# Optimization experiments

Hardware: AMD Instinct MI355X
Metric: run time of the kernel (lower is better)

## Reference

```python
import jax, jax.numpy as jnp
import numpy as np

BSZ, NW, T = 16, 1024, 3072   # batch, max words per seq, padded byte length
BED, WED = 128, 512           # byte_embed_dim, word_embed_dim
NH = 2                        # highway layers per block
VOCAB = 256 + 4 + 4
BPE_MASK_IDX = 4


def _conv1d(x, W, b):
    # x: [B, T, Cin], W: [k, Cin, Cout]
    y = jax.lax.conv_general_dilated(x, W, window_strides=(1,), padding='SAME',
                                     dimension_numbers=('NWC', 'WIO', 'NWC'))
    return y + b


def _highway(x, Ws, bs):
    # Ws: [NH, 2D, D], bs: [NH, 2D]; AllenNLP-style highway
    for i in range(NH):
        proj = x @ Ws[i].T + bs[i]
        h, g = jnp.split(proj, 2, axis=-1)
        g = jax.nn.sigmoid(g)
        x = g * jax.nn.relu(h) + (1.0 - g) * x
    return x


def setup_inputs() -> dict:
    rng = np.random.default_rng(0)
    pool_lengths = rng.integers(1, 4, size=(BSZ, NW)).astype(np.int64)  # all >=1 -> npools == NW
    src_lengths = pool_lengths.sum(axis=1)
    byte_tokens = np.zeros((BSZ, T), dtype=np.int64)
    for b in range(BSZ):
        L = int(src_lengths[b])
        byte_tokens[b, :L] = rng.integers(4, 260, size=L)
    pos = np.arange(T)[None, :]
    bpe_mask = (rng.random((BSZ, T)) < 0.3) & (pos < src_lengths[:, None])

    key = jax.random.key(0)
    ks = jax.random.split(key, 12)
    s = 0.02
    tok_emb = jax.random.normal(ks[0], (VOCAB, BED), jnp.float32) * s
    tok_emb = tok_emb.at[0].set(0.0)  # padding_idx = 0
    return {
        'byte_tokens': jnp.asarray(byte_tokens),
        'bpe_mask': jnp.asarray(bpe_mask),
        'pool_lengths': jnp.asarray(pool_lengths),
        'tok_emb': tok_emb,
        'conv0_W': jax.random.normal(ks[1], (3, BED, WED), jnp.float32) * s,
        'conv0_b': jnp.zeros((WED,), jnp.float32),
        'conv1_W': jax.random.normal(ks[2], (3, WED, WED), jnp.float32) * s,
        'conv1_b': jnp.zeros((WED,), jnp.float32),
        'hw0_W': jax.random.normal(ks[3], (NH, 2 * WED, WED), jnp.float32) * s,
        'hw0_b': jnp.zeros((NH, 2 * WED), jnp.float32),
        'hw1_W': jax.random.normal(ks[4], (NH, 2 * WED, WED), jnp.float32) * s,
        'hw1_b': jnp.zeros((NH, 2 * WED), jnp.float32),
        'proj_W': jax.random.normal(ks[5], (WED, WED), jnp.float32) * s,
        'proj_b': jnp.zeros((WED,), jnp.float32),
    }


def reference(byte_tokens, bpe_mask, pool_lengths, tok_emb,
              conv0_W, conv0_b, conv1_W, conv1_b,
              hw0_W, hw0_b, hw1_W, hw1_b, proj_W, proj_b):
    # byte embedding + bpe-marker embedding (index 0 row is zero => no-op where mask is False)
    x = tok_emb[byte_tokens] + tok_emb[jnp.where(bpe_mask, BPE_MASK_IDX, 0)]
    # ConvHighway block 0 (no residual)
    x = _highway(jax.nn.relu(_conv1d(x, conv0_W, conv0_b)), hw0_W, hw0_b)
    # ConvHighway block 1 (residual_conv=True); dropout is identity in eval
    x = _highway(jax.nn.relu(_conv1d(x, conv1_W, conv1_b)) + x, hw1_W, hw1_b)

    # ragged per-word max pool via segment_max (replaces the python double loop)
    cum = jnp.cumsum(pool_lengths, axis=1)                 # [B, NW]
    pos = jnp.arange(T)
    seg = jax.vmap(lambda c: jnp.searchsorted(c, pos, side='right'))(cum)  # [B, T]
    src_len = cum[:, -1]
    valid = pos[None, :] < src_len[:, None]
    gid = jnp.where(valid, jnp.arange(BSZ)[:, None] * NW + jnp.clip(seg, 0, NW - 1), BSZ * NW)
    pooled = jax.ops.segment_max(x.reshape(BSZ * T, WED), gid.reshape(-1),
                                 num_segments=BSZ * NW + 1)
    pooled = pooled[:BSZ * NW].reshape(BSZ, NW, WED)
    pooled = jnp.where(jnp.isfinite(pooled), pooled, 0.0)  # empty pools -> 0 like new_zeros
    return pooled @ proj_W.T + proj_b
```

## Files before the change

kernel.cpp:

```cpp
#include <hip/hip_runtime.h>
#include <hip/hip_bf16.h>
#include <math.h>

typedef __attribute__((ext_vector_type(8))) short short8v;
typedef __attribute__((ext_vector_type(4))) float float4v;

namespace {
constexpr int kBSZ = 16;
constexpr int kNW  = 1024;
constexpr int kT   = 3072;
constexpr int kBED = 128;
constexpr int kWED = 512;
constexpr int kR   = kBSZ * kT;
constexpr int kMP  = kBSZ * kNW;
}

__device__ __forceinline__ unsigned short f2b(float x) {
  unsigned int u = __float_as_uint(x);
  u = u + 0x7FFFu + ((u >> 16) & 1u);
  return (unsigned short)(u >> 16);
}
__device__ __forceinline__ float b2f(unsigned short u) {
  return __uint_as_float(((unsigned int)u) << 16);
}

__device__ __forceinline__ void async16(void* l, const void* g) {
  __builtin_amdgcn_global_load_lds(
      (const __attribute__((address_space(1))) void*)g,
      (__attribute__((address_space(3))) void*)l, 16, 0, 0);
}

__device__ __forceinline__ int swz(int row) { return (row >> 1) & 3; }

__global__ __launch_bounds__(256) void k_embed(
    const int* __restrict__ tok, const int* __restrict__ msk,
    const float* __restrict__ emb, unsigned short* __restrict__ out) {
  int idx = blockIdx.x * 256 + threadIdx.x;
  int row = idx >> 5, c4 = idx & 31;
  const float4* e4 = (const float4*)emb;
  float4 a = e4[tok[row] * 32 + c4];
  float4 b = e4[(msk[row] ? 4 : 0) * 32 + c4];
  ushort4 o;
  o.x = f2b(a.x + b.x); o.y = f2b(a.y + b.y);
  o.z = f2b(a.z + b.z); o.w = f2b(a.w + b.w);
  ((ushort4*)out)[idx] = o;
}

__global__ __launch_bounds__(256) void k_prep(
    const float* __restrict__ c0W, const float* __restrict__ c1W,
    const float* __restrict__ h0W, const float* __restrict__ h1W,
    const float* __restrict__ pW,
    unsigned short* __restrict__ cw0, unsigned short* __restrict__ cw1,
    unsigned short* __restrict__ hw0, unsigned short* __restrict__ hw1,
    unsigned short* __restrict__ pwb) {
  int idx = blockIdx.x * 256 + threadIdx.x;
  if (idx < 196608) {
    int k = idx & 127, n = (idx >> 7) & 511, dt = idx >> 16;
    cw0[idx] = f2b(c0W[(long)(dt * 128 + k) * 512 + n]);
    return;
  }
  idx -= 196608;
  if (idx < 786432) {
    int k = idx & 511, n = (idx >> 9) & 511, dt = idx >> 18;
    cw1[idx] = f2b(c1W[(long)(dt * 512 + k) * 512 + n]);
    return;
  }
  idx -= 786432;
  if (idx < 1048576) { hw0[idx] = f2b(h0W[idx]); return; }
  idx -= 1048576;
  if (idx < 1048576) { hw1[idx] = f2b(h1W[idx]); return; }
  idx -= 1048576;
  if (idx < 262144)  { pwb[idx] = f2b(pW[idx]); }
}

__global__ void k_cumsum(const int* __restrict__ pl, int* __restrict__ cum) {
  __shared__ int s[kNW];
  int b = blockIdx.x, i = threadIdx.x;
  s[i] = pl[b * kNW + i];
  __syncthreads();
  for (int off = 1; off < kNW; off <<= 1) {
    int cur = s[i];
    int add = (i >= off) ? s[i - off] : 0;
    __syncthreads();
    s[i] = cur + add;
    __syncthreads();
  }
  cum[b * kNW + i] = s[i];
}

template <int CIN, bool RESID>
__global__ __launch_bounds__(256, 2) void k_convm(
    const unsigned short* __restrict__ X,
    const unsigned short* __restrict__ Wt,
    const float* __restrict__ bias,
    const unsigned short* __restrict__ resid,
    const int* __restrict__ cum,
    unsigned short* __restrict__ out) {
  const int row0 = blockIdx.x * 128, n0 = blockIdx.y * 128;
  const int b = row0 / kT, t0 = row0 % kT;
  if (t0 >= cum[b * kNW + kNW - 1] + 2) return;

  constexpr int NT = CIN / 32;
  __shared__ short lds[2][(130 + 384) * 32];
  const int tid = threadIdx.x, wave = tid >> 6, lane = tid & 63;
  const int q = lane >> 4, rr = lane & 15;
  const int dr = lane >> 2, sl = lane & 3;
  const bool lo_ok = (t0 > 0), hi_ok = (t0 + 128 < kT);
  const int wr = (wave >> 1) * 64, wc = (wave & 1) * 64;

  float4v acc[4][4] = {};
  short8v hv = {0, 0, 0, 0, 0, 0, 0, 0};
  const int hch = tid & 3;
  const long hrow = (tid < 4) ? (long)(row0 - 1) : (long)(row0 + 128);
  const bool hok = (tid < 4) ? lo_ok : hi_ok;

  auto stage = [&](int nb, int k0) {
    short* As = lds[nb];
    short* Bs = lds[nb] + 130 * 32;
#pragma unroll
    for (int i = 0; i < 2; ++i) {
      int r0 = (wave + 4 * i) * 16;
      int ch = sl ^ swz(1 + r0 + dr);
      async16((char*)As + (1 + r0) * 64,
              X + (long)(row0 + r0 + dr) * CIN + k0 + ch * 8);
    }
#pragma unroll
    for (int i = 0; i < 6; ++i) {
      int r0 = (wave + 4 * i) * 16;
      int br = r0 + dr;
      int ch = sl ^ swz(br);
      int dt = br >> 7, n = br & 127;
      async16((char*)Bs + r0 * 64,
              Wt + ((long)(dt * kWED + n0 + n)) * CIN + k0 + ch * 8);
    }
    if (tid < 8) {
      short8v v = {0, 0, 0, 0, 0, 0, 0, 0};
      if (hok) v = *(const short8v*)(X + hrow * CIN + k0 + hch * 8);
      hv = v;
    }
  };
  auto halo_write = [&](int nb) {
    if (tid < 8) {
      int r = (tid < 4) ? 0 : 129;
      *(short8v*)((char*)lds[nb] + r * 64 + hch * 16) = hv;
    }
  };

  stage(0, 0);
  halo_write(0);
  __syncthreads();

  for (int t = 0; t < NT; ++t) {
    const int cur = t & 1, nb = cur ^ 1;
    if (t + 1 < NT) stage(nb, (t + 1) * 32);
    __builtin_amdgcn_sched_barrier(0);
    const char* As = (const char*)lds[cur];
    const char* Bs = (const char*)(lds[cur] + 130 * 32);
#pragma unroll
    for (int dt = 0; dt < 3; ++dt) {
      short8v a[4], bb[4];
#pragma unroll
      for (int mf = 0; mf < 4; ++mf) {
        int ra = wr + rr + dt + mf * 16;
        a[mf] = *(const short8v*)(As + ra * 64 + ((q ^ swz(ra)) * 16));
      }
#pragma unroll
      for (int nf = 0; nf < 4; ++nf) {
        int rb = dt * 128 + wc + rr + nf * 16;
        bb[nf] = *(const short8v*)(Bs + rb * 64 + ((q ^ swz(rb)) * 16));
      }
#pragma unroll
      for (int mf = 0; mf < 4; ++mf)
#pragma unroll
        for (int nf = 0; nf < 4; ++nf)
          acc[mf][nf] = __builtin_amdgcn_mfma_f32_16x16x32_bf16(
              a[mf], bb[nf], acc[mf][nf], 0, 0, 0);
    }
    if (t + 1 < NT) halo_write(nb);
    __syncthreads();
  }

#pragma unroll
  for (int nf = 0; nf < 4; ++nf) {
    int col = n0 + wc + nf * 16 + rr;
    float bv = bias[col];
#pragma unroll
    for (int mf = 0; mf < 4; ++mf)
#pragma unroll
      for (int r = 0; r < 4; ++r) {
        long row = row0 + wr + mf * 16 + q * 4 + r;
        float y = fmaxf(acc[mf][nf][r] + bv, 0.f);
        if (RESID) y += b2f(resid[row * kWED + col]);
        out[row * kWED + col] = f2b(y);
      }
  }
}

__global__ __launch_bounds__(256, 2) void k_hw(
    const unsigned short* __restrict__ X,
    const unsigned short* __restrict__ Wb,
    const float* __restrict__ bias,
    const int* __restrict__ cum,
    unsigned short* __restrict__ out) {
  const int row0 = blockIdx.x * 128, n0 = blockIdx.y * 128;
  const int b = row0 / kT, t0 = row0 % kT;
  if (t0 >= cum[b * kNW + kNW - 1] + 2) return;

  __shared__ short lds[2][(128 + 256) * 32];
  const int tid = threadIdx.x, wave = tid >> 6, lane = tid & 63;
  const int q = lane >> 4, rr = lane & 15;
  const int dr = lane >> 2, sl = lane & 3;
  const int wr = (wave >> 1) * 64, wc = (wave & 1) * 64;

  float4v acch[4][4] = {}, accg[4][4] = {};

  auto stage = [&](int nb, int k0) {
    short* As = lds[nb];
    short* Bs = lds[nb] + 128 * 32;
#pragma unroll
    for (int i = 0; i < 2; ++i) {
      int r0 = (wave + 4 * i) * 16;
      int ch = sl ^ swz(r0 + dr);
      async16((char*)As + r0 * 64,
              X + (long)(row0 + r0 + dr) * kWED + k0 + ch * 8);
    }
#pragma unroll
    for (int i = 0; i < 4; ++i) {
      int r0 = (wave + 4 * i) * 16;
      int br = r0 + dr;
      int ch = sl ^ swz(br);
      int g = br >> 7, n = br & 127;
      async16((char*)Bs + r0 * 64,
              Wb + ((long)(g * 512 + n0 + n)) * kWED + k0 + ch * 8);
    }
  };

  stage(0, 0);
  __syncthreads();

  for (int t = 0; t < 16; ++t) {
    const int cur = t & 1, nb = cur ^ 1;
    if (t + 1 < 16) stage(nb, (t + 1) * 32);
    __builtin_amdgcn_sched_barrier(0);
    const char* As = (const char*)lds[cur];
    const char* Bs = (const char*)(lds[cur] + 128 * 32);
    short8v a[4], bh[4], bg[4];
#pragma unroll
    for (int mf = 0; mf < 4; ++mf) {
      int ra = wr + rr + mf * 16;
      a[mf] = *(const short8v*)(As + ra * 64 + ((q ^ swz(ra)) * 16));
    }
#pragma unroll
    for (int nf = 0; nf < 4; ++nf) {
      int rh = wc + rr + nf * 16;
      int rg = 128 + rh;
      bh[nf] = *(const short8v*)(Bs + rh * 64 + ((q ^ swz(rh)) * 16));
      bg[nf] = *(const short8v*)(Bs + rg * 64 + ((q ^ swz(rg)) * 16));
    }
#pragma unroll
    for (int mf = 0; mf < 4; ++mf)
#pragma unroll
      for (int nf = 0; nf < 4; ++nf) {
        acch[mf][nf] = __builtin_amdgcn_mfma_f32_16x16x32_bf16(
            a[mf], bh[nf], acch[mf][nf], 0, 0, 0);
        accg[mf][nf] = __builtin_amdgcn_mfma_f32_16x16x32_bf16(
            a[mf], bg[nf], accg[mf][nf], 0, 0, 0);
      }
    __syncthreads();
  }

#pragma unroll
  for (int nf = 0; nf < 4; ++nf) {
    int col = n0 + wc + nf * 16 + rr;
    float bhv = bias[col], bgv = bias[512 + col];
#pragma unroll
    for (int mf = 0; mf < 4; ++mf)
#pragma unroll
      for (int r = 0; r < 4; ++r) {
        long row = row0 + wr + mf * 16 + q * 4 + r;
        float h = fmaxf(acch[mf][nf][r] + bhv, 0.f);
        float g = 1.f / (1.f + __expf(-(accg[mf][nf][r] + bgv)));
        float xv = b2f(X[row * kWED + col]);
        out[row * kWED + col] = f2b(g * h + (1.f - g) * xv);
      }
  }
}

__global__ __launch_bounds__(256, 2) void k_proj(
    const unsigned short* __restrict__ A,
    const unsigned short* __restrict__ Wb,
    const float* __restrict__ bias,
    float* __restrict__ out) {
  __shared__ short lds[2][(128 + 128) * 32];
  const int tid = threadIdx.x, wave = tid >> 6, lane = tid & 63;
  const int q = lane >> 4, rr = lane & 15;
  const int dr = lane >> 2, sl = lane & 3;
  const int row0 = blockIdx.x * 128, n0 = blockIdx.y * 128;
  const int wr = (wave >> 1) * 64, wc = (wave & 1) * 64;

  float4v acc[4][4] = {};

  auto stage = [&](int nb, int k0) {
    short* As = lds[nb];
    short* Bs = lds[nb] + 128 * 32;
#pragma unroll
    for (int i = 0; i < 2; ++i) {
      int r0 = (wave + 4 * i) * 16;
      int ch = sl ^ swz(r0 + dr);
      async16((char*)As + r0 * 64,
              A + (long)(row0 + r0 + dr) * kWED + k0 + ch * 8);
    }
#pragma unroll
    for (int i = 0; i < 2; ++i) {
      int r0 = (wave + 4 * i) * 16;
      int ch = sl ^ swz(r0 + dr);
      async16((char*)Bs + r0 * 64,
              Wb + (long)(n0 + r0 + dr) * kWED + k0 + ch * 8);
    }
  };

  stage(0, 0);
  __syncthreads();

  for (int t = 0; t < 16; ++t) {
    const int cur = t & 1, nb = cur ^ 1;
    if (t + 1 < 16) stage(nb, (t + 1) * 32);
    __builtin_amdgcn_sched_barrier(0);
    const char* As = (const char*)lds[cur];
    const char* Bs = (const char*)(lds[cur] + 128 * 32);
    short8v a[4], bb[4];
#pragma unroll
    for (int mf = 0; mf < 4; ++mf) {
      int ra = wr + rr + mf * 16;
      a[mf] = *(const short8v*)(As + ra * 64 + ((q ^ swz(ra)) * 16));
    }
#pragma unroll
    for (int nf = 0; nf < 4; ++nf) {
      int rb = wc + rr + nf * 16;
      bb[nf] = *(const short8v*)(Bs + rb * 64 + ((q ^ swz(rb)) * 16));
    }
#pragma unroll
    for (int mf = 0; mf < 4; ++mf)
#pragma unroll
      for (int nf = 0; nf < 4; ++nf)
        acc[mf][nf] = __builtin_amdgcn_mfma_f32_16x16x32_bf16(
            a[mf], bb[nf], acc[mf][nf], 0, 0, 0);
    __syncthreads();
  }

#pragma unroll
  for (int nf = 0; nf < 4; ++nf) {
    int col = n0 + wc + nf * 16 + rr;
    float bv = bias[col];
#pragma unroll
    for (int mf = 0; mf < 4; ++mf)
#pragma unroll
      for (int r = 0; r < 4; ++r) {
        long row = row0 + wr + mf * 16 + q * 4 + r;
        out[row * kWED + col] = acc[mf][nf][r] + bv;
      }
  }
}

__global__ __launch_bounds__(128) void k_pool(
    const unsigned short* __restrict__ x, const int* __restrict__ cum,
    unsigned short* __restrict__ pooled) {
  int bw = blockIdx.x;
  int b = bw >> 10, w = bw & 1023;
  int s = (w == 0) ? 0 : cum[bw - 1];
  int e = cum[bw];
  int c = threadIdx.x;
  float m0 = -INFINITY, m1 = -INFINITY, m2 = -INFINITY, m3 = -INFINITY;
  for (int t = s; t < e; ++t) {
    ushort4 v = ((const ushort4*)(x + (long)(b * kT + t) * kWED))[c];
    m0 = fmaxf(m0, b2f(v.x)); m1 = fmaxf(m1, b2f(v.y));
    m2 = fmaxf(m2, b2f(v.z)); m3 = fmaxf(m3, b2f(v.w));
  }
  if (e <= s) { m0 = m1 = m2 = m3 = 0.f; }
  ushort4 o;
  o.x = f2b(m0); o.y = f2b(m1); o.z = f2b(m2); o.w = f2b(m3);
  ((ushort4*)(pooled + (long)bw * kWED))[c] = o;
}

extern "C" void kernel_launch(void* const* d_in, const int* in_sizes, int n_in,
                              void* d_out, int out_size, void* d_ws, size_t ws_size,
                              hipStream_t stream) {
  (void)in_sizes; (void)n_in; (void)out_size; (void)ws_size;

  const int*   tok = (const int*)d_in[0];
  const int*   msk = (const int*)d_in[1];
  const int*   pl  = (const int*)d_in[2];
  const float* emb = (const float*)d_in[3];
  const float* c0W = (const float*)d_in[4];
  const float* c0b = (const float*)d_in[5];
  const float* c1W = (const float*)d_in[6];
  const float* c1b = (const float*)d_in[7];
  const float* h0W = (const float*)d_in[8];
  const float* h0b = (const float*)d_in[9];
  const float* h1W = (const float*)d_in[10];
  const float* h1b = (const float*)d_in[11];
  const float* pW  = (const float*)d_in[12];
  const float* pb  = (const float*)d_in[13];

  unsigned short* xb0 = (unsigned short*)d_ws;
  unsigned short* xb1 = xb0 + (size_t)kR * kWED;
  unsigned short* cw0 = xb1 + (size_t)kR * kWED;
  unsigned short* cw1 = cw0 + 3 * kWED * kBED;
  unsigned short* hw0 = cw1 + 3 * kWED * kWED;
  unsigned short* hw1 = hw0 + 2 * 1024 * kWED;
  unsigned short* pwb = hw1 + 2 * 1024 * kWED;
  int* cum = (int*)(pwb + kWED * kWED);

  k_cumsum<<<kBSZ, kNW, 0, stream>>>(pl, cum);

  k_prep<<<(3342336 + 255) / 256, 256, 0, stream>>>(
      c0W, c1W, h0W, h1W, pW, cw0, cw1, hw0, hw1, pwb);

  k_embed<<<kR * 32 / 256, 256, 0, stream>>>(tok, msk, emb, xb0);

  dim3 g1(kR / 128, kWED / 128);

  k_convm<kBED, false><<<g1, 256, 0, stream>>>(xb0, cw0, c0b, nullptr, cum, xb1);
  k_hw<<<g1, 256, 0, stream>>>(xb1, hw0, h0b, cum, xb0);
  k_hw<<<g1, 256, 0, stream>>>(xb0, hw0 + 1024 * kWED, h0b + 1024, cum, xb1);
  k_convm<kWED, true><<<g1, 256, 0, stream>>>(xb1, cw1, c1b, xb1, cum, xb0);
  k_hw<<<g1, 256, 0, stream>>>(xb0, hw1, h1b, cum, xb1);
  k_hw<<<g1, 256, 0, stream>>>(xb1, hw1 + 1024 * kWED, h1b + 1024, cum, xb0);

  k_pool<<<kMP, 128, 0, stream>>>(xb0, cum, xb1);

  dim3 g2(kMP / 128, kWED / 128);
  k_proj<<<g2, 256, 0, stream>>>(xb1, pwb, pb, (float*)d_out);
}
```

Baseline: 399.8 us.

## Triple-buffer highway and projection GEMM LDS pipelines with explicit vmcnt waits

Switches the highway and projection GEMM kernels from double to triple buffering in LDS, prefetching two K-steps ahead. Each stage is issued after the current tile's LDS reads, and the loop waits with partial vmcnt counts plus a raw s_barrier instead of a full __syncthreads. The aim is to hide global-load latency behind the MFMA work. In exchange, LDS use per block grows by half (about 72 KB for k_hw), which may cut the number of resident blocks, and correctness depends on the hand-counted vmcnt values.

```diff
diff --git a/kernel.cpp b/kernel.cpp
--- a/kernel.cpp
+++ b/kernel.cpp
@@ -4,6 +4,9 @@
 
 typedef __attribute__((ext_vector_type(8))) short short8v;
 typedef __attribute__((ext_vector_type(4))) float float4v;
+
+#define VMCNT(n) asm volatile("s_waitcnt vmcnt(" #n ")" ::: "memory")
+#define LGK0     asm volatile("s_waitcnt lgkmcnt(0)" ::: "memory")
 
 namespace {
 constexpr int kBSZ = 16;
@@ -206,7 +209,7 @@
   const int b = row0 / kT, t0 = row0 % kT;
   if (t0 >= cum[b * kNW + kNW - 1] + 2) return;
 
-  __shared__ short lds[2][(128 + 256) * 32];
+  __shared__ short lds[3][(128 + 256) * 32];
   const int tid = threadIdx.x, wave = tid >> 6, lane = tid & 63;
   const int q = lane >> 4, rr = lane & 15;
   const int dr = lane >> 2, sl = lane & 3;
@@ -236,14 +239,14 @@
   };
 
   stage(0, 0);
-  __syncthreads();
+  stage(1, 32);
+  VMCNT(6);
+  __builtin_amdgcn_s_barrier();
+  __builtin_amdgcn_sched_barrier(0);
 
   for (int t = 0; t < 16; ++t) {
-    const int cur = t & 1, nb = cur ^ 1;
-    if (t + 1 < 16) stage(nb, (t + 1) * 32);
-    __builtin_amdgcn_sched_barrier(0);
-    const char* As = (const char*)lds[cur];
-    const char* Bs = (const char*)(lds[cur] + 128 * 32);
+    const char* As = (const char*)lds[t % 3];
+    const char* Bs = (const char*)(lds[t % 3] + 128 * 32);
     short8v a[4], bh[4], bg[4];
 #pragma unroll
     for (int mf = 0; mf < 4; ++mf) {
@@ -257,6 +260,8 @@
       bh[nf] = *(const short8v*)(Bs + rh * 64 + ((q ^ swz(rh)) * 16));
       bg[nf] = *(const short8v*)(Bs + rg * 64 + ((q ^ swz(rg)) * 16));
     }
+    if (t + 2 < 16) stage((t + 2) % 3, (t + 2) * 32);
+    LGK0; __builtin_amdgcn_sched_barrier(0);
 #pragma unroll
     for (int mf = 0; mf < 4; ++mf)
 #pragma unroll
@@ -266,7 +271,9 @@
         accg[mf][nf] = __builtin_amdgcn_mfma_f32_16x16x32_bf16(
             a[mf], bg[nf], accg[mf][nf], 0, 0, 0);
       }
-    __syncthreads();
+    if (t + 2 < 16) { VMCNT(6); } else { VMCNT(0); }
+    __builtin_amdgcn_s_barrier();
+    __builtin_amdgcn_sched_barrier(0);
   }
 
 #pragma unroll
@@ -291,7 +298,7 @@
     const unsigned short* __restrict__ Wb,
     const float* __restrict__ bias,
     float* __restrict__ out) {
-  __shared__ short lds[2][(128 + 128) * 32];
+  __shared__ short lds[3][(128 + 128) * 32];
   const int tid = threadIdx.x, wave = tid >> 6, lane = tid & 63;
   const int q = lane >> 4, rr = lane & 15;
   const int dr = lane >> 2, sl = lane & 3;
@@ -320,14 +327,14 @@
   };
 
   stage(0, 0);
-  __syncthreads();
+  stage(1, 32);
+  VMCNT(4);
+  __builtin_amdgcn_s_barrier();
+  __builtin_amdgcn_sched_barrier(0);
 
   for (int t = 0; t < 16; ++t) {
-    const int cur = t & 1, nb = cur ^ 1;
-    if (t + 1 < 16) stage(nb, (t + 1) * 32);
-    __builtin_amdgcn_sched_barrier(0);
-    const char* As = (const char*)lds[cur];
-    const char* Bs = (const char*)(lds[cur] + 128 * 32);
+    const char* As = (const char*)lds[t % 3];
+    const char* Bs = (const char*)(lds[t % 3] + 128 * 32);
     short8v a[4], bb[4];
 #pragma unroll
     for (int mf = 0; mf < 4; ++mf) {
@@ -339,13 +346,17 @@
       int rb = wc + rr + nf * 16;
       bb[nf] = *(const short8v*)(Bs + rb * 64 + ((q ^ swz(rb)) * 16));
     }
+    if (t + 2 < 16) stage((t + 2) % 3, (t + 2) * 32);
+    LGK0; __builtin_amdgcn_sched_barrier(0);
 #pragma unroll
     for (int mf = 0; mf < 4; ++mf)
 #pragma unroll
       for (int nf = 0; nf < 4; ++nf)
         acc[mf][nf] = __builtin_amdgcn_mfma_f32_16x16x32_bf16(
             a[mf], bb[nf], acc[mf][nf], 0, 0, 0);
-    __syncthreads();
+    if (t + 2 < 16) { VMCNT(4); } else { VMCNT(0); }
+    __builtin_amdgcn_s_barrier();
+    __builtin_amdgcn_sched_barrier(0);
   }
 
 #pragma unroll
```

Result: no change. 398.4 us (-0.4%).

## Single-buffer LDS in GEMM kernels and raise occupancy via launch bounds

Applied to the files above, without the earlier changes.

Drops the double-buffered LDS prefetch pipeline in the conv, highway and projection GEMM kernels in favour of a single buffer with load-sync-compute-sync per K step. It also precomputes incrementing global pointers and raises the launch-bounds occupancy targets. The aim is to fit more blocks per CU so wave-level parallelism hides memory latency. In exchange it loses intra-block overlap of loads with MFMA and puts more pressure on registers.

```diff
diff --git a/kernel.cpp b/kernel.cpp
--- a/kernel.cpp
+++ b/kernel.cpp
@@ -89,7 +89,7 @@
 }
 
 template <int CIN, bool RESID>
-__global__ __launch_bounds__(256, 2) void k_convm(
+__global__ __launch_bounds__(256, 4) void k_convm(
     const unsigned short* __restrict__ X,
     const unsigned short* __restrict__ Wt,
     const float* __restrict__ bias,
@@ -101,7 +101,7 @@
   if (t0 >= cum[b * kNW + kNW - 1] + 2) return;
 
   constexpr int NT = CIN / 32;
-  __shared__ short lds[2][(130 + 384) * 32];
+  __shared__ short lds[(130 + 384) * 32];
   const int tid = threadIdx.x, wave = tid >> 6, lane = tid & 63;
   const int q = lane >> 4, rr = lane & 15;
   const int dr = lane >> 2, sl = lane & 3;
@@ -109,53 +109,48 @@
   const int wr = (wave >> 1) * 64, wc = (wave & 1) * 64;
 
   float4v acc[4][4] = {};
-  short8v hv = {0, 0, 0, 0, 0, 0, 0, 0};
+
+  const unsigned short* pA[2];
+  int lA[2];
+#pragma unroll
+  for (int i = 0; i < 2; ++i) {
+    int r0 = (wave + 4 * i) * 16;
+    int ch = sl ^ swz(1 + r0 + dr);
+    pA[i] = X + (long)(row0 + r0 + dr) * CIN + ch * 8;
+    lA[i] = (1 + r0) * 64;
+  }
+  const unsigned short* pB[6];
+  int lB[6];
+#pragma unroll
+  for (int i = 0; i < 6; ++i) {
+    int r0 = (wave + 4 * i) * 16;
+    int br = r0 + dr;
+    int ch = sl ^ swz(br);
+    int dt = br >> 7, n = br & 127;
+    pB[i] = Wt + ((long)(dt * kWED + n0 + n)) * CIN + ch * 8;
+    lB[i] = (130 + r0) * 64;
+  }
   const int hch = tid & 3;
   const long hrow = (tid < 4) ? (long)(row0 - 1) : (long)(row0 + 128);
   const bool hok = (tid < 4) ? lo_ok : hi_ok;
-
-  auto stage = [&](int nb, int k0) {
-    short* As = lds[nb];
-    short* Bs = lds[nb] + 130 * 32;
-#pragma unroll
-    for (int i = 0; i < 2; ++i) {
-      int r0 = (wave + 4 * i) * 16;
-      int ch = sl ^ swz(1 + r0 + dr);
-      async16((char*)As + (1 + r0) * 64,
-              X + (long)(row0 + r0 + dr) * CIN + k0 + ch * 8);
-    }
-#pragma unroll
-    for (int i = 0; i < 6; ++i) {
-      int r0 = (wave + 4 * i) * 16;
-      int br = r0 + dr;
-      int ch = sl ^ swz(br);
-      int dt = br >> 7, n = br & 127;
-      async16((char*)Bs + r0 * 64,
-              Wt + ((long)(dt * kWED + n0 + n)) * CIN + k0 + ch * 8);
-    }
+  const unsigned short* pH = X + hrow * CIN + hch * 8;
+  const int lH = ((tid < 4) ? 0 : 129) * 64 + hch * 16;
+
+  for (int t = 0; t < NT; ++t) {
+#pragma unroll
+    for (int i = 0; i < 2; ++i) { async16((char*)lds + lA[i], pA[i]); pA[i] += 32; }
+#pragma unroll
+    for (int i = 0; i < 6; ++i) { async16((char*)lds + lB[i], pB[i]); pB[i] += 32; }
     if (tid < 8) {
       short8v v = {0, 0, 0, 0, 0, 0, 0, 0};
-      if (hok) v = *(const short8v*)(X + hrow * CIN + k0 + hch * 8);
-      hv = v;
-    }
-  };
-  auto halo_write = [&](int nb) {
-    if (tid < 8) {
-      int r = (tid < 4) ? 0 : 129;
-      *(short8v*)((char*)lds[nb] + r * 64 + hch * 16) = hv;
-    }
-  };
-
-  stage(0, 0);
-  halo_write(0);
-  __syncthreads();
-
-  for (int t = 0; t < NT; ++t) {
-    const int cur = t & 1, nb = cur ^ 1;
-    if (t + 1 < NT) stage(nb, (t + 1) * 32);
-    __builtin_amdgcn_sched_barrier(0);
-    const char* As = (const char*)lds[cur];
-    const char* Bs = (const char*)(lds[cur] + 130 * 32);
+      if (hok) v = *(const short8v*)pH;
+      *(short8v*)((char*)lds + lH) = v;
+    }
+    pH += 32;
+    __syncthreads();
+
+    const char* As = (const char*)lds;
+    const char* Bs = (const char*)(lds + 130 * 32);
 #pragma unroll
     for (int dt = 0; dt < 3; ++dt) {
       short8v a[4], bb[4];
@@ -176,7 +171,6 @@
           acc[mf][nf] = __builtin_amdgcn_mfma_f32_16x16x32_bf16(
               a[mf], bb[nf], acc[mf][nf], 0, 0, 0);
     }
-    if (t + 1 < NT) halo_write(nb);
     __syncthreads();
   }
 
@@ -196,7 +190,7 @@
   }
 }
 
-__global__ __launch_bounds__(256, 2) void k_hw(
+__global__ __launch_bounds__(256, 3) void k_hw(
     const unsigned short* __restrict__ X,
     const unsigned short* __restrict__ Wb,
     const float* __restrict__ bias,
@@ -206,7 +200,7 @@
   const int b = row0 / kT, t0 = row0 % kT;
   if (t0 >= cum[b * kNW + kNW - 1] + 2) return;
 
-  __shared__ short lds[2][(128 + 256) * 32];
+  __shared__ short lds[(128 + 256) * 32];
   const int tid = threadIdx.x, wave = tid >> 6, lane = tid & 63;
   const int q = lane >> 4, rr = lane & 15;
   const int dr = lane >> 2, sl = lane & 3;
@@ -214,37 +208,37 @@
 
   float4v acch[4][4] = {}, accg[4][4] = {};
 
-  auto stage = [&](int nb, int k0) {
-    short* As = lds[nb];
-    short* Bs = lds[nb] + 128 * 32;
-#pragma unroll
-    for (int i = 0; i < 2; ++i) {
-      int r0 = (wave + 4 * i) * 16;
-      int ch = sl ^ swz(r0 + dr);
-      async16((char*)As + r0 * 64,
-              X + (long)(row0 + r0 + dr) * kWED + k0 + ch * 8);
-    }
-#pragma unroll
-    for (int i = 0; i < 4; ++i) {
-      int r0 = (wave + 4 * i) * 16;
-      int br = r0 + dr;
-      int ch = sl ^ swz(br);
-      int g = br >> 7, n = br & 127;
-      async16((char*)Bs + r0 * 64,
-              Wb + ((long)(g * 512 + n0 + n)) * kWED + k0 + ch * 8);
-    }
-  };
-
-  stage(0, 0);
-  __syncthreads();
+  const unsigned short* pA[2];
+  int lA[2];
+#pragma unroll
+  for (int i = 0; i < 2; ++i) {
+    int r0 = (wave + 4 * i) * 16;
+    int ch = sl ^ swz(r0 + dr);
+    pA[i] = X + (long)(row0 + r0 + dr) * kWED + ch * 8;
+    lA[i] = r0 * 64;
+  }
+  const unsigned short* pB[4];
+  int lB[4];
+#pragma unroll
+  for (int i = 0; i < 4; ++i) {
+    int r0 = (wave + 4 * i) * 16;
+    int br = r0 + dr;
+    int ch = sl ^ swz(br);
+    int g = br >> 7, n = br & 127;
+    pB[i] = Wb + ((long)(g * 512 + n0 + n)) * kWED + ch * 8;
+    lB[i] = (128 + r0) * 64;
+  }
 
   for (int t = 0; t < 16; ++t) {
-    const int cur = t & 1, nb = cur ^ 1;
-    if (t + 1 < 16) stage(nb, (t + 1) * 32);
-    __builtin_amdgcn_sched_barrier(0);
-    const char* As = (const char*)lds[cur];
-    const char* Bs = (const char*)(lds[cur] + 128 * 32);
-    short8v a[4], bh[4], bg[4];
+#pragma unroll
+    for (int i = 0; i < 2; ++i) { async16((char*)lds + lA[i], pA[i]); pA[i] += 32; }
+#pragma unroll
+    for (int i = 0; i < 4; ++i) { async16((char*)lds + lB[i], pB[i]); pB[i] += 32; }
+    __syncthreads();
+
+    const char* As = (const char*)lds;
+    const char* Bs = (const char*)(lds + 128 * 32);
+    short8v a[4];
 #pragma unroll
     for (int mf = 0; mf < 4; ++mf) {
       int ra = wr + rr + mf * 16;
@@ -254,18 +248,16 @@
     for (int nf = 0; nf < 4; ++nf) {
       int rh = wc + rr + nf * 16;
       int rg = 128 + rh;
-      bh[nf] = *(const short8v*)(Bs + rh * 64 + ((q ^ swz(rh)) * 16));
-      bg[nf] = *(const short8v*)(Bs + rg * 64 + ((q ^ swz(rg)) * 16));
-    }
-#pragma unroll
-    for (int mf = 0; mf < 4; ++mf)
-#pragma unroll
-      for (int nf = 0; nf < 4; ++nf) {
+      short8v bh = *(const short8v*)(Bs + rh * 64 + ((q ^ swz(rh)) * 16));
+      short8v bg = *(const short8v*)(Bs + rg * 64 + ((q ^ swz(rg)) * 16));
+#pragma unroll
+      for (int mf = 0; mf < 4; ++mf) {
         acch[mf][nf] = __builtin_amdgcn_mfma_f32_16x16x32_bf16(
-            a[mf], bh[nf], acch[mf][nf], 0, 0, 0);
+            a[mf], bh, acch[mf][nf], 0, 0, 0);
         accg[mf][nf] = __builtin_amdgcn_mfma_f32_16x16x32_bf16(
-            a[mf], bg[nf], accg[mf][nf], 0, 0, 0);
-      }
+            a[mf], bg, accg[mf][nf], 0, 0, 0);
+      }
+    }
     __syncthreads();
   }
 
@@ -286,12 +278,12 @@
   }
 }
 
-__global__ __launch_bounds__(256, 2) void k_proj(
+__global__ __launch_bounds__(256, 4) void k_proj(
     const unsigned short* __restrict__ A,
     const unsigned short* __restrict__ Wb,
     const float* __restrict__ bias,
     float* __restrict__ out) {
-  __shared__ short lds[2][(128 + 128) * 32];
+  __shared__ short lds[(128 + 128) * 32];
   const int tid = threadIdx.x, wave = tid >> 6, lane = tid & 63;
   const int q = lane >> 4, rr = lane & 15;
   const int dr = lane >> 2, sl = lane & 3;
@@ -300,34 +292,28 @@
 
   float4v acc[4][4] = {};
 
-  auto stage = [&](int nb, int k0) {
-    short* As = lds[nb];
-    short* Bs = lds[nb] + 128 * 32;
-#pragma unroll
-    for (int i = 0; i < 2; ++i) {
-      int r0 = (wave + 4 * i) * 16;
-      int ch = sl ^ swz(r0 + dr);
-      async16((char*)As + r0 * 64,
-              A + (long)(row0 + r0 + dr) * kWED + k0 + ch * 8);
-    }
-#pragma unroll
-    for (int i = 0; i < 2; ++i) {
-      int r0 = (wave + 4 * i) * 16;
-      int ch = sl ^ swz(r0 + dr);
-      async16((char*)Bs + r0 * 64,
-              Wb + (long)(n0 + r0 + dr) * kWED + k0 + ch * 8);
-    }
-  };
-
-  stage(0, 0);
-  __syncthreads();
+  const unsigned short* pA[2];
+  const unsigned short* pB[2];
+  int lA[2], lB[2];
+#pragma unroll
+  for (int i = 0; i < 2; ++i) {
+    int r0 = (wave + 4 * i) * 16;
+    int ch = sl ^ swz(r0 + dr);
+    pA[i] = A + (long)(row0 + r0 + dr) * kWED + ch * 8;
+    lA[i] = r0 * 64;
+    pB[i] = Wb + (long)(n0 + r0 + dr) * kWED + ch * 8;
+    lB[i] = (128 + r0) * 64;
+  }
 
   for (int t = 0; t < 16; ++t) {
-    const int cur = t & 1, nb = cur ^ 1;
-    if (t + 1 < 16) stage(nb, (t + 1) * 32);
-    __builtin_amdgcn_sched_barrier(0);
-    const char* As = (const char*)lds[cur];
-    const char* Bs = (const char*)(lds[cur] + 128 * 32);
+#pragma unroll
+    for (int i = 0; i < 2; ++i) { async16((char*)lds + lA[i], pA[i]); pA[i] += 32; }
+#pragma unroll
+    for (int i = 0; i < 2; ++i) { async16((char*)lds + lB[i], pB[i]); pB[i] += 32; }
+    __syncthreads();
+
+    const char* As = (const char*)lds;
+    const char* Bs = (const char*)(lds + 128 * 32);
     short8v a[4], bb[4];
 #pragma unroll
     for (int mf = 0; mf < 4; ++mf) {
```

Measured after the change: 674.0 us. 68.6% more time.
